# Performance work log

Measured on AMD Instinct MI355X. Metric: run time of the kernel, lower is better.

## Reference

```python
import jax, jax.numpy as jnp
import numpy as np

N = 50000        # nodes
E = 800000       # edges
F_IN = 32        # float features (x also carries 1 trailing cell-id column)
CELL_DIM = 16
NUM_CELLS = 854
C = 64           # out_channels
H0, H1 = 2, 1    # heads schedule for num_layers=2 -> [2, 1]
D_IN = F_IN + CELL_DIM  # 48, GAT input dim after cell embedding concat
NEG_SLOPE = 0.2  # PyG GATConv default negative_slope


def setup_inputs() -> dict:
    key = jax.random.key(0)
    ks = jax.random.split(key, 14)
    base = jax.random.normal(ks[0], (N, F_IN), jnp.float32)
    cell_ids = jax.random.randint(ks[1], (N,), 0, NUM_CELLS)
    x = jnp.concatenate([base, cell_ids.astype(jnp.float32)[:, None]], axis=1)
    edge_index = jax.random.randint(ks[2], (2, E), 0, N, dtype=jnp.int32)
    s = lambda f: 1.0 / np.sqrt(f)
    emb = jax.random.normal(ks[3], (NUM_CELLS, CELL_DIM), jnp.float32)
    W0 = jax.random.normal(ks[4], (D_IN, H0 * C), jnp.float32) * s(D_IN)
    a_src0 = jax.random.normal(ks[5], (H0, C), jnp.float32) * s(C)
    a_dst0 = jax.random.normal(ks[6], (H0, C), jnp.float32) * s(C)
    b0 = jnp.zeros((C,), jnp.float32)
    ln_g = jnp.ones((C,), jnp.float32)
    ln_b = jnp.zeros((C,), jnp.float32)
    W1 = jax.random.normal(ks[7], (C, H1 * C), jnp.float32) * s(C)
    a_src1 = jax.random.normal(ks[8], (H1, C), jnp.float32) * s(C)
    a_dst1 = jax.random.normal(ks[9], (H1, C), jnp.float32) * s(C)
    b1 = jnp.zeros((C,), jnp.float32)
    return {"x": x, "edge_index": edge_index, "emb": emb,
            "W0": W0, "a_src0": a_src0, "a_dst0": a_dst0, "b0": b0,
            "ln_g": ln_g, "ln_b": ln_b,
            "W1": W1, "a_src1": a_src1, "a_dst1": a_dst1, "b1": b1}


def gat_layer(h_in, src, dst, W, a_src, a_dst, b, heads):
    # h_in: [N, D]; src/dst: [E'] (self-loops already appended)
    h = (h_in @ W).reshape(N, heads, C)                 # [N, H, C]
    alpha_s = jnp.einsum('nhc,hc->nh', h, a_src)        # [N, H]
    alpha_d = jnp.einsum('nhc,hc->nh', h, a_dst)
    e = jax.nn.leaky_relu(alpha_s[src] + alpha_d[dst], NEG_SLOPE)  # [E', H]
    # segment softmax over incoming edges of each dst node
    m = jax.ops.segment_max(e, dst, num_segments=N)     # [N, H]
    ex = jnp.exp(e - m[dst])
    denom = jax.ops.segment_sum(ex, dst, num_segments=N)
    alpha = ex / denom[dst]                             # [E', H]
    msg = h[src] * alpha[:, :, None]                    # [E', H, C]
    out = jax.ops.segment_sum(msg, dst, num_segments=N) # [N, H, C]
    return out.mean(axis=1) + b                         # concat=False -> mean over heads


def layer_norm(x, g, b):
    mu = x.mean(-1, keepdims=True)
    var = ((x - mu) ** 2).mean(-1, keepdims=True)
    return (x - mu) * jax.lax.rsqrt(var + 1e-5) * g + b


def reference(x, edge_index, emb, W0, a_src0, a_dst0, b0, ln_g, ln_b,
              W1, a_src1, a_dst1, b1):
    base = x[:, :-1]
    cell_ids = x[:, -1].astype(jnp.int32)
    h = jnp.concatenate([base, emb[cell_ids]], axis=1)  # [N, 48]
    # add self-loops (PyG GATConv default add_self_loops=True)
    loop = jnp.arange(N, dtype=edge_index.dtype)
    src = jnp.concatenate([edge_index[0], loop])
    dst = jnp.concatenate([edge_index[1], loop])
    h = gat_layer(h, src, dst, W0, a_src0, a_dst0, b0, H0)
    h = jax.nn.elu(layer_norm(h, ln_g, ln_b))           # dropout is identity at eval
    h = gat_layer(h, src, dst, W1, a_src1, a_dst1, b1, H1)
    return h
```

## Files before the change

### kernel.cpp

```cpp
#include <hip/hip_runtime.h>
#include <hip/hip_bf16.h>

#define N_NODES 50000
#define N_EDGES 800000
#define F_IN 32
#define CELL_DIM 16
#define D_IN 48
#define X_STRIDE 33
#define NUM_CELLS 854
#define NEG_SLOPE 0.2f
#define NODE0_BLOCKS 2048
#define MERGE_BLOCKS 1563
#define EDGE_BLOCKS 3125
#define NXCD 8
#define BWX 16
#define BW 48
#define W 24

typedef unsigned int uint;
typedef unsigned short ushort;

static __device__ __forceinline__ uint f2b(float f) {
  uint x = __float_as_uint(f);
  return (x + 0x7fffu + ((x >> 16) & 1u)) >> 16;
}
static __device__ __forceinline__ float b2f_lo(uint w) { return __uint_as_float(w << 16); }
static __device__ __forceinline__ float b2f_hi(uint w) { return __uint_as_float(w & 0xffff0000u); }
static __device__ __forceinline__ float lrelu(float e) { return fmaxf(e, NEG_SLOPE * e); }


__global__ __launch_bounds__(256) void k_bfill(const int* __restrict__ ei,
                                               int* __restrict__ cnt,
                                               ushort* __restrict__ bkt) {
  int e = blockIdx.x * 256 + threadIdx.x;
  if (e >= N_EDGES) return;
  uint xcc;
  asm volatile("s_getreg_b32 %0, hwreg(HW_REG_XCC_ID)" : "=s"(xcc));
  xcc &= (NXCD - 1);
  int s = ei[e], d = ei[N_EDGES + e];
  int p = atomicAdd(&cnt[xcc * N_NODES + d], 1);
  if (p < BWX) bkt[(xcc * N_NODES + d) * BWX + p] = (ushort)s;
}


__global__ __launch_bounds__(256) void k_merge(const int* __restrict__ cnt,
                                               const ushort* __restrict__ bkt,
                                               int* __restrict__ cntc,
                                               ushort* __restrict__ bktc) {
  int tid = threadIdx.x;
  int n = blockIdx.x * 32 + (tid >> 3);
  if (n >= N_NODES) return;
  int xg = tid & 7;
  int cx = min(cnt[xg * N_NODES + n], BWX);
  int sc = cx;
#pragma unroll
  for (int o = 1; o < 8; o <<= 1) {
    int t = __shfl_up(sc, o, 64);
    if ((tid & 7) >= o) sc += t;
  }
  int total = __shfl(sc, (tid & 63) | 7, 64);
  int base = sc - cx;
  const ushort* src = bkt + (xg * N_NODES + n) * BWX;
  for (int k = 0; k < cx; ++k) {
    int slot = base + k;
    if (slot < BW) bktc[n * BW + slot] = src[k];
  }
  if (xg == 7) cntc[n] = min(total, BW);
}


__global__ __launch_bounds__(256) void k_node0(const float* __restrict__ x,
                                               const float* __restrict__ emb,
                                               const float* __restrict__ W0,
                                               const float* __restrict__ asrc,
                                               const float* __restrict__ adst,
                                               ushort* __restrict__ h0u,
                                               float* __restrict__ as0, float* __restrict__ ad0) {
  int tid = threadIdx.x;
  __shared__ float hin[8][48];
  int lane = tid & 63, wid = tid >> 6;
  int h = wid & 1;
  int q = wid >> 1;
  float w0r[D_IN];
#pragma unroll
  for (int k = 0; k < D_IN; ++k) w0r[k] = W0[k * 128 + h * 64 + lane];
  float av_s = asrc[h * 64 + lane], av_d = adst[h * 64 + lane];

  for (int g = blockIdx.x; g < N_NODES / 8; g += NODE0_BLOCKS) {
    int nb = g * 8;
#pragma unroll
    for (int j = 0; j < 2; ++j) {
      int loc = 2 * wid + j;
      int n = nb + loc;
      float t = 0.f;
      if (lane < 33) t = x[n * X_STRIDE + lane];
      int cid = (int)__shfl(t, 32, 64);
      cid = cid < 0 ? 0 : (cid >= NUM_CELLS ? NUM_CELLS - 1 : cid);
      if (lane >= 32 && lane < 48) t = emb[cid * CELL_DIM + (lane - 32)];
      if (lane < 48) hin[loc][lane] = t;
    }
    __syncthreads();
#pragma unroll
    for (int j = 0; j < 4; ++j) {
      int loc = 4 * q + j;
      int n = nb + loc;
      const float4* hp = (const float4*)hin[loc];
      float acc = 0.f;
#pragma unroll
      for (int k4 = 0; k4 < 12; ++k4) {
        float4 hh = hp[k4];
        acc = fmaf(hh.x, w0r[4 * k4 + 0], acc);
        acc = fmaf(hh.y, w0r[4 * k4 + 1], acc);
        acc = fmaf(hh.z, w0r[4 * k4 + 2], acc);
        acc = fmaf(hh.w, w0r[4 * k4 + 3], acc);
      }
      h0u[(n * 64 + lane) * 2 + h] = (ushort)f2b(acc);
      float sa = acc * av_s, sd = acc * av_d;
#pragma unroll
      for (int o = 32; o >= 1; o >>= 1) {
        sa += __shfl_xor(sa, o, 64);
        sd += __shfl_xor(sd, o, 64);
      }
      if (lane == 0) {
        as0[n * 2 + h] = sa;
        ad0[n * 2 + h] = sd;
      }
    }
    __syncthreads();
  }
}


__global__ __launch_bounds__(256) void k_agg0(const int* __restrict__ cnt,
                                              const ushort* __restrict__ bkt,
                                              const float2* __restrict__ as0v,
                                              const float2* __restrict__ ad0v,
                                              const uint* __restrict__ h0p,
                                              const float* __restrict__ b0,
                                              const float* __restrict__ lng,
                                              const float* __restrict__ lnb,
                                              const float* __restrict__ W1,
                                              const float* __restrict__ asrc1,
                                              const float* __restrict__ adst1,
                                              ushort* __restrict__ h1b,
                                              float* __restrict__ as1, float* __restrict__ ad1) {
  __shared__ uint gbuf[4][W * 64];
  __shared__ float yb[4][64];
  int tid = threadIdx.x;
  int lane = tid & 63, wl = tid >> 6;
  int n = blockIdx.x * 4 + wl;
  int nE = cnt[n];
  int items = nE + 1;
  float2 ad = ad0v[n];
  float acc0 = 0.f, acc1 = 0.f, den0 = 0.f, den1 = 0.f;
  uint* gb = gbuf[wl];

  for (int w0 = 0; w0 < items; w0 += W) {
    int idx = w0 + lane;
    uint s = 0u;
    float wv0 = 0.f, wv1 = 0.f;
    if (lane < W && idx < items) {
      s = (idx < nE) ? (uint)bkt[n * BW + idx] : (uint)n;
      float2 a = as0v[s];
      wv0 = __expf(lrelu(a.x + ad.x));
      wv1 = __expf(lrelu(a.y + ad.y));
    }
#pragma unroll
    for (int j = 0; j < W; ++j) {
      uint sx = (uint)__builtin_amdgcn_readlane((int)s, j);
      __builtin_amdgcn_global_load_lds((const uint*)(h0p + sx * 64u + (uint)lane),
                                       gb + j * 64, 4, 0, 0);
    }
    asm volatile("s_waitcnt vmcnt(0)" ::: "memory");
    __builtin_amdgcn_sched_barrier(0);
#pragma unroll
    for (int j = 0; j < W; ++j) {
      float w0j = __uint_as_float(
          (uint)__builtin_amdgcn_readlane((int)__float_as_uint(wv0), j));
      float w1j = __uint_as_float(
          (uint)__builtin_amdgcn_readlane((int)__float_as_uint(wv1), j));
      uint h = gb[j * 64 + lane];
      acc0 = fmaf(w0j, b2f_lo(h), acc0); den0 += w0j;
      acc1 = fmaf(w1j, b2f_hi(h), acc1); den1 += w1j;
    }
    asm volatile("s_waitcnt lgkmcnt(0)" ::: "memory");
    __builtin_amdgcn_sched_barrier(0);
  }

  float v = 0.5f * (acc0 / den0 + acc1 / den1) + b0[lane];
  float mu = v;
#pragma unroll
  for (int o = 32; o >= 1; o >>= 1) mu += __shfl_xor(mu, o, 64);
  mu *= (1.0f / 64.0f);
  float d = v - mu;
  float vr = d * d;
#pragma unroll
  for (int o = 32; o >= 1; o >>= 1) vr += __shfl_xor(vr, o, 64);
  vr *= (1.0f / 64.0f);
  float y = d * rsqrtf(vr + 1e-5f) * lng[lane] + lnb[lane];
  y = y > 0.f ? y : expm1f(y);
  yb[wl][lane] = y;
  const float4* yp = (const float4*)yb[wl];
  float q0 = 0.f, q1 = 0.f, q2 = 0.f, q3 = 0.f;
#pragma unroll
  for (int k4 = 0; k4 < 16; ++k4) {
    float4 yy = yp[k4];
    q0 = fmaf(yy.x, W1[(4 * k4 + 0) * 64 + lane], q0);
    q1 = fmaf(yy.y, W1[(4 * k4 + 1) * 64 + lane], q1);
    q2 = fmaf(yy.z, W1[(4 * k4 + 2) * 64 + lane], q2);
    q3 = fmaf(yy.w, W1[(4 * k4 + 3) * 64 + lane], q3);
  }
  float h1v = (q0 + q1) + (q2 + q3);
  h1b[n * 64 + lane] = (ushort)f2b(h1v);
  float sa = h1v * asrc1[lane];
  float sdv = h1v * adst1[lane];
#pragma unroll
  for (int o = 32; o >= 1; o >>= 1) {
    sa += __shfl_xor(sa, o, 64);
    sdv += __shfl_xor(sdv, o, 64);
  }
  if (lane == 0) {
    as1[n] = sa;
    ad1[n] = sdv;
  }
}


__global__ __launch_bounds__(256) void k_agg1(const int* __restrict__ cnt,
                                              const ushort* __restrict__ bkt,
                                              const ushort* __restrict__ h1b,
                                              const float* __restrict__ as1,
                                              const float* __restrict__ ad1,
                                              const float* __restrict__ b1,
                                              float* __restrict__ out) {
  __shared__ uint gbuf[4][W * 64];
  int tid = threadIdx.x;
  int lane = tid & 63, wl = tid >> 6;
  int n = blockIdx.x * 4 + wl;
  int nE = cnt[n];
  int items = nE + 1;
  float adv = ad1[n];
  float acc = 0.f, den = 0.f;
  uint* gb = gbuf[wl];
  const ushort* gbs = (const ushort*)gb;

  for (int w0 = 0; w0 < items; w0 += W) {
    int idx = w0 + lane;
    uint s = 0u;
    float wv = 0.f;
    if (lane < W && idx < items) {
      s = (idx < nE) ? (uint)bkt[n * BW + idx] : (uint)n;
      wv = __expf(lrelu(as1[s] + adv));
    }
    uint hl = lane & 31;
#pragma unroll
    for (int j = 0; j < W; ++j) {
      uint sx = (uint)__builtin_amdgcn_readlane((int)s, j);
      __builtin_amdgcn_global_load_lds((const uint*)(h1b + sx * 64u) + hl,
                                       gb + j * 64, 4, 0, 0);
    }
    asm volatile("s_waitcnt vmcnt(0)" ::: "memory");
    __builtin_amdgcn_sched_barrier(0);
#pragma unroll
    for (int j = 0; j < W; ++j) {
      float wj = __uint_as_float(
          (uint)__builtin_amdgcn_readlane((int)__float_as_uint(wv), j));
      uint hh = (uint)gbs[j * 128 + lane];
      acc = fmaf(wj, __uint_as_float(hh << 16), acc);
      den += wj;
    }
    asm volatile("s_waitcnt lgkmcnt(0)" ::: "memory");
    __builtin_amdgcn_sched_barrier(0);
  }
  out[n * 64 + lane] = acc / den + b1[lane];
}


extern "C" void kernel_launch(void* const* d_in, const int* in_sizes, int n_in,
                              void* d_out, int out_size, void* d_ws, size_t ws_size,
                              hipStream_t stream) {
  const float* x    = (const float*)d_in[0];
  const int*   ei   = (const int*)d_in[1];
  const float* emb  = (const float*)d_in[2];
  const float* W0   = (const float*)d_in[3];
  const float* as0w = (const float*)d_in[4];
  const float* ad0w = (const float*)d_in[5];
  const float* b0   = (const float*)d_in[6];
  const float* lng  = (const float*)d_in[7];
  const float* lnb  = (const float*)d_in[8];
  const float* W1   = (const float*)d_in[9];
  const float* as1w = (const float*)d_in[10];
  const float* ad1w = (const float*)d_in[11];
  const float* b1   = (const float*)d_in[12];
  float* out = (float*)d_out;

  ushort* bkt = (ushort*)d_ws;
  int* cnt    = (int*)(bkt + NXCD * N_NODES * BWX);
  ushort* bktc = (ushort*)(cnt + NXCD * N_NODES);
  int* cntc   = (int*)(bktc + N_NODES * BW);
  float* as0 = (float*)(cntc + N_NODES);
  float* ad0 = as0 + N_NODES * 2;
  float* as1 = ad0 + N_NODES * 2;
  float* ad1 = as1 + N_NODES;
  uint* h0p  = (uint*)(ad1 + N_NODES);
  ushort* h1b = (ushort*)(h0p + N_NODES * 64);

  hipMemsetAsync(cnt, 0, NXCD * N_NODES * sizeof(int), stream);
  k_bfill<<<EDGE_BLOCKS, 256, 0, stream>>>(ei, cnt, bkt);
  k_merge<<<MERGE_BLOCKS, 256, 0, stream>>>(cnt, bkt, cntc, bktc);
  k_node0<<<NODE0_BLOCKS, 256, 0, stream>>>(x, emb, W0, as0w, ad0w, (ushort*)h0p, as0, ad0);
  k_agg0<<<N_NODES / 4, 256, 0, stream>>>(cntc, bktc, (const float2*)as0, (const float2*)ad0,
                                          h0p, b0, lng, lnb, W1, as1w, ad1w, h1b, as1, ad1);
  k_agg1<<<N_NODES / 4, 256, 0, stream>>>(cntc, bktc, h1b, as1, ad1, b1, out);
}
```

Baseline: 257.4 us.

## Precompute layer-0 attention weights in merge and pack two neighbors per agg1 load

Moves k_merge after k_node0 so it can compute the two-head exp(leaky_relu) edge weights, pack them as bf16 pairs, and store them next to each source index as uint2 records. k_agg0 then reads these precomputed weights instead of gathering as0 and computing exps per edge. k_agg1 splits the wave into two half-waves that each fetch a different neighbor's 32-word bf16 row, which halves the number of LDS-DMA load instructions. The workspace is also reordered so h1b and as1/ad1 reuse the dead bucket and count buffers. The cost is bf16 rounding of attention weights and wider 8-byte bucket records.

```diff
diff --git a/kernel.cpp b/kernel.cpp
--- a/kernel.cpp
+++ b/kernel.cpp
@@ -16,6 +16,7 @@
 #define BWX 16
 #define BW 48
 #define W 24
+#define NP 12
 
 typedef unsigned int uint;
 typedef unsigned short ushort;
@@ -40,32 +41,6 @@
   int s = ei[e], d = ei[N_EDGES + e];
   int p = atomicAdd(&cnt[xcc * N_NODES + d], 1);
   if (p < BWX) bkt[(xcc * N_NODES + d) * BWX + p] = (ushort)s;
-}
-
-
-__global__ __launch_bounds__(256) void k_merge(const int* __restrict__ cnt,
-                                               const ushort* __restrict__ bkt,
-                                               int* __restrict__ cntc,
-                                               ushort* __restrict__ bktc) {
-  int tid = threadIdx.x;
-  int n = blockIdx.x * 32 + (tid >> 3);
-  if (n >= N_NODES) return;
-  int xg = tid & 7;
-  int cx = min(cnt[xg * N_NODES + n], BWX);
-  int sc = cx;
-#pragma unroll
-  for (int o = 1; o < 8; o <<= 1) {
-    int t = __shfl_up(sc, o, 64);
-    if ((tid & 7) >= o) sc += t;
-  }
-  int total = __shfl(sc, (tid & 63) | 7, 64);
-  int base = sc - cx;
-  const ushort* src = bkt + (xg * N_NODES + n) * BWX;
-  for (int k = 0; k < cx; ++k) {
-    int slot = base + k;
-    if (slot < BW) bktc[n * BW + slot] = src[k];
-  }
-  if (xg == 7) cntc[n] = min(total, BW);
 }
 
 
@@ -131,8 +106,40 @@
 }
 
 
-__global__ __launch_bounds__(256) void k_agg0(const int* __restrict__ cnt,
-                                              const ushort* __restrict__ bkt,
+__global__ __launch_bounds__(256) void k_merge(const int* __restrict__ cnt,
+                                               const ushort* __restrict__ bkt,
+                                               const float2* __restrict__ as0v,
+                                               const float2* __restrict__ ad0v,
+                                               int* __restrict__ cntc,
+                                               uint2* __restrict__ bktw) {
+  int tid = threadIdx.x;
+  int n = blockIdx.x * 32 + (tid >> 3);
+  if (n >= N_NODES) return;
+  int xg = tid & 7;
+  int cx = min(cnt[xg * N_NODES + n], BWX);
+  int sc = cx;
+#pragma unroll
+  for (int o = 1; o < 8; o <<= 1) {
+    int t = __shfl_up(sc, o, 64);
+    if ((tid & 7) >= o) sc += t;
+  }
+  int total = __shfl(sc, (tid & 63) | 7, 64);
+  int base = sc - cx;
+  float2 ad = ad0v[n];
+  const ushort* src = bkt + (xg * N_NODES + n) * BWX;
+  for (int k = 0; k < cx; ++k) {
+    uint s = src[k];
+    float2 a = as0v[s];
+    uint wp = f2b(__expf(lrelu(a.x + ad.x))) | (f2b(__expf(lrelu(a.y + ad.y))) << 16);
+    int slot = base + k;
+    if (slot < BW) bktw[n * BW + slot] = make_uint2(s, wp);
+  }
+  if (xg == 7) cntc[n] = min(total, BW);
+}
+
+
+__global__ __launch_bounds__(256) void k_agg0(const int* __restrict__ cntc,
+                                              const uint2* __restrict__ bktw,
                                               const float2* __restrict__ as0v,
                                               const float2* __restrict__ ad0v,
                                               const uint* __restrict__ h0p,
@@ -149,25 +156,22 @@
   int tid = threadIdx.x;
   int lane = tid & 63, wl = tid >> 6;
   int n = blockIdx.x * 4 + wl;
-  int nE = cnt[n];
+  int nE = cntc[n];
   int items = nE + 1;
+  float2 a_n = as0v[n];
   float2 ad = ad0v[n];
+  uint selfw = f2b(__expf(lrelu(a_n.x + ad.x))) | (f2b(__expf(lrelu(a_n.y + ad.y))) << 16);
   float acc0 = 0.f, acc1 = 0.f, den0 = 0.f, den1 = 0.f;
   uint* gb = gbuf[wl];
 
   for (int w0 = 0; w0 < items; w0 += W) {
     int idx = w0 + lane;
-    uint s = 0u;
-    float wv0 = 0.f, wv1 = 0.f;
-    if (lane < W && idx < items) {
-      s = (idx < nE) ? (uint)bkt[n * BW + idx] : (uint)n;
-      float2 a = as0v[s];
-      wv0 = __expf(lrelu(a.x + ad.x));
-      wv1 = __expf(lrelu(a.y + ad.y));
-    }
+    uint2 rec = make_uint2(0u, 0u);
+    if (lane < W && idx < items)
+      rec = (idx < nE) ? bktw[n * BW + idx] : make_uint2((uint)n, selfw);
 #pragma unroll
     for (int j = 0; j < W; ++j) {
-      uint sx = (uint)__builtin_amdgcn_readlane((int)s, j);
+      uint sx = (uint)__builtin_amdgcn_readlane((int)rec.x, j);
       __builtin_amdgcn_global_load_lds((const uint*)(h0p + sx * 64u + (uint)lane),
                                        gb + j * 64, 4, 0, 0);
     }
@@ -175,13 +179,11 @@
     __builtin_amdgcn_sched_barrier(0);
 #pragma unroll
     for (int j = 0; j < W; ++j) {
-      float w0j = __uint_as_float(
-          (uint)__builtin_amdgcn_readlane((int)__float_as_uint(wv0), j));
-      float w1j = __uint_as_float(
-          (uint)__builtin_amdgcn_readlane((int)__float_as_uint(wv1), j));
+      uint wy = (uint)__builtin_amdgcn_readlane((int)rec.y, j);
       uint h = gb[j * 64 + lane];
-      acc0 = fmaf(w0j, b2f_lo(h), acc0); den0 += w0j;
-      acc1 = fmaf(w1j, b2f_hi(h), acc1); den1 += w1j;
+      float w;
+      w = b2f_lo(wy); acc0 += w * b2f_lo(h); den0 += w;
+      w = b2f_hi(wy); acc1 += w * b2f_hi(h); den1 += w;
     }
     asm volatile("s_waitcnt lgkmcnt(0)" ::: "memory");
     __builtin_amdgcn_sched_barrier(0);
@@ -226,48 +228,56 @@
 }
 
 
-__global__ __launch_bounds__(256) void k_agg1(const int* __restrict__ cnt,
-                                              const ushort* __restrict__ bkt,
+__global__ __launch_bounds__(256) void k_agg1(const int* __restrict__ cntc,
+                                              const uint2* __restrict__ bktw,
                                               const ushort* __restrict__ h1b,
                                               const float* __restrict__ as1,
                                               const float* __restrict__ ad1,
                                               const float* __restrict__ b1,
                                               float* __restrict__ out) {
-  __shared__ uint gbuf[4][W * 64];
+  __shared__ uint gbuf[4][NP * 64];
   int tid = threadIdx.x;
   int lane = tid & 63, wl = tid >> 6;
   int n = blockIdx.x * 4 + wl;
-  int nE = cnt[n];
+  int nE = cntc[n];
   int items = nE + 1;
   float adv = ad1[n];
   float acc = 0.f, den = 0.f;
   uint* gb = gbuf[wl];
   const ushort* gbs = (const ushort*)gb;
+  uint hl = lane & 31;
+  int half = lane >> 5;
 
   for (int w0 = 0; w0 < items; w0 += W) {
     int idx = w0 + lane;
     uint s = 0u;
     float wv = 0.f;
     if (lane < W && idx < items) {
-      s = (idx < nE) ? (uint)bkt[n * BW + idx] : (uint)n;
+      s = (idx < nE) ? bktw[n * BW + idx].x : (uint)n;
       wv = __expf(lrelu(as1[s] + adv));
     }
-    uint hl = lane & 31;
-#pragma unroll
-    for (int j = 0; j < W; ++j) {
-      uint sx = (uint)__builtin_amdgcn_readlane((int)s, j);
-      __builtin_amdgcn_global_load_lds((const uint*)(h1b + sx * 64u) + hl,
+#pragma unroll
+    for (int j = 0; j < NP; ++j) {
+      uint sxA = (uint)__builtin_amdgcn_readlane((int)s, 2 * j);
+      uint sxB = (uint)__builtin_amdgcn_readlane((int)s, 2 * j + 1);
+      uint sx2 = half ? sxB : sxA;
+      __builtin_amdgcn_global_load_lds((const uint*)(h1b + sx2 * 64u) + hl,
                                        gb + j * 64, 4, 0, 0);
     }
     asm volatile("s_waitcnt vmcnt(0)" ::: "memory");
     __builtin_amdgcn_sched_barrier(0);
 #pragma unroll
-    for (int j = 0; j < W; ++j) {
-      float wj = __uint_as_float(
-          (uint)__builtin_amdgcn_readlane((int)__float_as_uint(wv), j));
-      uint hh = (uint)gbs[j * 128 + lane];
-      acc = fmaf(wj, __uint_as_float(hh << 16), acc);
-      den += wj;
+    for (int j = 0; j < NP; ++j) {
+      float wA = __uint_as_float(
+          (uint)__builtin_amdgcn_readlane((int)__float_as_uint(wv), 2 * j));
+      float wB = __uint_as_float(
+          (uint)__builtin_amdgcn_readlane((int)__float_as_uint(wv), 2 * j + 1));
+      uint hA = (uint)gbs[j * 128 + lane];
+      uint hB = (uint)gbs[j * 128 + 64 + lane];
+      acc = fmaf(wA, __uint_as_float(hA << 16), acc);
+      den += wA;
+      acc = fmaf(wB, __uint_as_float(hB << 16), acc);
+      den += wB;
     }
     asm volatile("s_waitcnt lgkmcnt(0)" ::: "memory");
     __builtin_amdgcn_sched_barrier(0);
@@ -294,22 +304,23 @@
   const float* b1   = (const float*)d_in[12];
   float* out = (float*)d_out;
 
-  ushort* bkt = (ushort*)d_ws;
-  int* cnt    = (int*)(bkt + NXCD * N_NODES * BWX);
-  ushort* bktc = (ushort*)(cnt + NXCD * N_NODES);
-  int* cntc   = (int*)(bktc + N_NODES * BW);
-  float* as0 = (float*)(cntc + N_NODES);
-  float* ad0 = as0 + N_NODES * 2;
-  float* as1 = ad0 + N_NODES * 2;
-  float* ad1 = as1 + N_NODES;
-  uint* h0p  = (uint*)(ad1 + N_NODES);
-  ushort* h1b = (ushort*)(h0p + N_NODES * 64);
+  ushort* bkt  = (ushort*)d_ws;
+  ushort* h1b  = (ushort*)d_ws;
+  int*    cnt  = (int*)((char*)d_ws + (size_t)NXCD * N_NODES * BWX * 2);
+  float*  as1  = (float*)cnt;
+  float*  ad1  = as1 + N_NODES;
+  uint2*  bktw = (uint2*)((char*)cnt + (size_t)NXCD * N_NODES * 4);
+  int*    cntc = (int*)(bktw + (size_t)N_NODES * BW);
+  float*  as0  = (float*)(cntc + N_NODES);
+  float*  ad0  = as0 + N_NODES * 2;
+  uint*   h0p  = (uint*)(ad0 + N_NODES * 2);
 
   hipMemsetAsync(cnt, 0, NXCD * N_NODES * sizeof(int), stream);
   k_bfill<<<EDGE_BLOCKS, 256, 0, stream>>>(ei, cnt, bkt);
-  k_merge<<<MERGE_BLOCKS, 256, 0, stream>>>(cnt, bkt, cntc, bktc);
   k_node0<<<NODE0_BLOCKS, 256, 0, stream>>>(x, emb, W0, as0w, ad0w, (ushort*)h0p, as0, ad0);
-  k_agg0<<<N_NODES / 4, 256, 0, stream>>>(cntc, bktc, (const float2*)as0, (const float2*)ad0,
+  k_merge<<<MERGE_BLOCKS, 256, 0, stream>>>(cnt, bkt, (const float2*)as0, (const float2*)ad0,
+                                            cntc, bktw);
+  k_agg0<<<N_NODES / 4, 256, 0, stream>>>(cntc, bktw, (const float2*)as0, (const float2*)ad0,
                                           h0p, b0, lng, lnb, W1, as1w, ad1w, h1b, as1, ad1);
-  k_agg1<<<N_NODES / 4, 256, 0, stream>>>(cntc, bktc, h1b, as1, ad1, b1, out);
-}
+  k_agg1<<<N_NODES / 4, 256, 0, stream>>>(cntc, bktw, h1b, as1, ad1, b1, out);
+}
```

New measurement: 252.8 us. No clear change (-1.8%).
